# Kernel tuning notes

Hardware: AMD Instinct MI355X
Metric: run time of the kernel (lower is better)

The kernel has to match this reference:

```python
import jax, jax.numpy as jnp
import numpy as np

INPUT_DIM = 1024
OUTPUT_DIM = 1024
DEGREE = 3


def setup_inputs() -> dict:
    key = jax.random.key(0)
    kx, kc = jax.random.split(key)
    x = jax.random.normal(kx, (8192, INPUT_DIM), dtype=jnp.float32)
    std = 1.0 / (INPUT_DIM * (DEGREE + 1))
    bessel_coeffs = std * jax.random.normal(kc, (INPUT_DIM, OUTPUT_DIM, DEGREE + 1), dtype=jnp.float32)
    return {"x": x, "bessel_coeffs": bessel_coeffs}


def reference(x, bessel_coeffs):
    # x: [B, I]; bessel_coeffs: [I, O, D+1]
    degree = bessel_coeffs.shape[-1] - 1
    x = jnp.tanh(x.reshape(-1, bessel_coeffs.shape[0]))
    # Bessel-polynomial-like recurrence: b0 = 1, b1 = x + 1,
    # b_i = (2i-1)*x*b_{i-1} + b_{i-2}
    basis = [jnp.ones_like(x)]
    if degree > 0:
        basis.append(x + 1.0)
    for i in range(2, degree + 1):
        basis.append((2 * i - 1) * x * basis[i - 1] + basis[i - 2])
    bessel = jnp.stack(basis, axis=-1)  # [B, I, D+1]
    y = jnp.einsum("bid,iod->bo", bessel, bessel_coeffs)
    return y
```

## Files before the change

### kernel.cpp

```cpp
#include <hip/hip_runtime.h>
#include <hip/hip_bf16.h>
#include <cstdint>
#include <cstddef>


#define BATCH   8192
#define IN_DIM  1024
#define OUT_DIM 1024
#define KB      3072
#define NT      24
#define BM      128
#define BN      128
#define BUFB    32768

#define SA1 56.307f
#define SA2 127.0f
#define SA3 124.534f
#define TB1 12783.33f
#define TB2 5667.68f
#define TB3 5779.91f
#define INV_S 1.389284e-6f

typedef __attribute__((ext_vector_type(4))) int   i32x4;

static __device__ __forceinline__ int q8(float v) {
    int q = __float2int_rn(v);
    return q < -127 ? -127 : (q > 127 ? 127 : q);
}

__global__ __launch_bounds__(256) void prep_basis(const float* __restrict__ x,
                                                  int8_t* __restrict__ Aq) {
    int idx = blockIdx.x * 256 + threadIdx.x;
    int b = idx >> 8;
    int i = (idx & 255) << 2;
    const float4 xv = *reinterpret_cast<const float4*>(&x[(size_t)b * IN_DIM + i]);
    float xs[4] = {xv.x, xv.y, xv.z, xv.w};
    int w1 = 0, w2 = 0, w3 = 0;
#pragma unroll
    for (int j = 0; j < 4; ++j) {
        float t  = tanhf(xs[j]);
        float t2 = t * t;
        float t3 = t2 * t;
        w1 |= (q8(SA1 * t)  & 0xff) << (8 * j);
        w2 |= (q8(SA2 * t2) & 0xff) << (8 * j);
        w3 |= (q8(SA3 * t3) & 0xff) << (8 * j);
    }
    int* row = (int*)(Aq + (size_t)b * KB);
    int c = i >> 2;
    row[c]       = w1;
    row[256 + c] = w2;
    row[512 + c] = w3;
}

__global__ __launch_bounds__(256) void prep_coeffs(const float* __restrict__ C,
                                                   int8_t* __restrict__ Bq,
                                                   float* __restrict__ bias) {
    __shared__ int8_t tile[3][32][33];
    __shared__ float red[8][32];
    const int i0 = blockIdx.x * 32;
    const int o0 = blockIdx.y * 32;
    const int t  = threadIdx.x;
    const int lo = t & 31;
    const int li = t >> 5;
    float part = 0.0f;
#pragma unroll
    for (int r = 0; r < 4; ++r) {
        int i = li + r * 8;
        const float4 c4 = *reinterpret_cast<const float4*>(
            &C[((size_t)(i0 + i) * OUT_DIM + (o0 + lo)) * 4]);
        tile[0][i][lo] = (int8_t)q8(TB1 * (c4.y + 3.0f * c4.z + 6.0f * c4.w));
        tile[1][i][lo] = (int8_t)q8(TB2 * (3.0f * c4.z + 15.0f * c4.w));
        tile[2][i][lo] = (int8_t)q8(TB3 * (15.0f * c4.w));
        part += c4.x + c4.y + c4.z + c4.w;
    }
    red[li][lo] = part;
    __syncthreads();
#pragma unroll
    for (int r = 0; r < 4; ++r) {
        int o = (t >> 5) + r * 8;
        int i = t & 31;
#pragma unroll
        for (int d = 0; d < 3; ++d)
            Bq[(size_t)(o0 + o) * KB + d * IN_DIM + (i0 + i)] = tile[d][i][o];
    }
    if (t < 32) {
        float s = 0.0f;
#pragma unroll
        for (int k = 0; k < 8; ++k) s += red[k][t];
        atomicAdd(&bias[o0 + t], s);
    }
}

__global__ __launch_bounds__(256, 2) void gemm_kan(
    const int8_t* __restrict__ Aq,
    const int8_t* __restrict__ Bq,
    const float* __restrict__ bias,
    float* __restrict__ out)
{
    extern __shared__ char smem[];

    const int tid  = threadIdx.x;
    const int lane = tid & 63;
    const int wid  = tid >> 6;
    const int wm   = wid >> 1;
    const int wn   = wid & 1;

    const int bid  = blockIdx.x;
    const int xcd  = bid & 7;
    const int j    = bid >> 3;
    const int brow = ((xcd >> 1) * 16 + (j >> 2)) * BM;
    const int bcol = ((xcd & 1) * 4 + (j & 3)) * BN;

    const int l15 = lane & 15, lh = lane >> 4, l7 = lane & 7;
    const int pc0 = lh ^ l7;
    const int pc1 = pc0 ^ 4;

    int aoff[4][2], boff[4][2];
#pragma unroll
    for (int mi = 0; mi < 4; ++mi) {
        int r = wm * 64 + mi * 16 + l15;
        aoff[mi][0] = r * 128 + pc0 * 16;
        aoff[mi][1] = r * 128 + pc1 * 16;
    }
#pragma unroll
    for (int ni = 0; ni < 4; ++ni) {
        int r = wn * 64 + ni * 16 + l15;
        boff[ni][0] = 16384 + r * 128 + pc0 * 16;
        boff[ni][1] = 16384 + r * 128 + pc1 * 16;
    }

    const int srow   = tid >> 3;
    const int schunk = (tid & 7) ^ (srow & 7);

#define STAGE(KT_TILE, P)                                                             \
    do {                                                                              \
        const int kt_ = (KT_TILE) * 128;                                              \
        char* lbase_ = smem + (P) * BUFB;                                             \
        _Pragma("unroll")                                                             \
        for (int s_ = 0; s_ < 4; ++s_) {                                              \
            __builtin_amdgcn_global_load_lds(                                         \
                (const __attribute__((address_space(1))) void*)(                      \
                    Aq + (size_t)(brow + s_ * 32 + srow) * KB + kt_ + schunk * 16),   \
                (__attribute__((address_space(3))) void*)(                            \
                    lbase_ + s_ * 4096 + tid * 16), 16, 0, 0);                        \
        }                                                                             \
        _Pragma("unroll")                                                             \
        for (int s_ = 0; s_ < 4; ++s_) {                                              \
            __builtin_amdgcn_global_load_lds(                                         \
                (const __attribute__((address_space(1))) void*)(                      \
                    Bq + (size_t)(bcol + s_ * 32 + srow) * KB + kt_ + schunk * 16),   \
                (__attribute__((address_space(3))) void*)(                            \
                    lbase_ + 16384 + s_ * 4096 + tid * 16), 16, 0, 0);                \
        }                                                                             \
    } while (0)

    i32x4 acc[4][4];
#pragma unroll
    for (int mi = 0; mi < 4; ++mi)
#pragma unroll
        for (int ni = 0; ni < 4; ++ni)
            acc[mi][ni] = (i32x4){0, 0, 0, 0};

    STAGE(0, 0);
    __syncthreads();

    for (int t = 0; t < NT; ++t) {
        const int p = t & 1;
        if (t + 1 < NT) STAGE(t + 1, p ^ 1);

        const char* lb = smem + p * BUFB;
        i32x4 af[4][2], bfr[4][2];
#pragma unroll
        for (int mi = 0; mi < 4; ++mi) {
            af[mi][0] = *reinterpret_cast<const i32x4*>(lb + aoff[mi][0]);
            af[mi][1] = *reinterpret_cast<const i32x4*>(lb + aoff[mi][1]);
        }
#pragma unroll
        for (int ni = 0; ni < 4; ++ni) {
            bfr[ni][0] = *reinterpret_cast<const i32x4*>(lb + boff[ni][0]);
            bfr[ni][1] = *reinterpret_cast<const i32x4*>(lb + boff[ni][1]);
        }
        __builtin_amdgcn_s_setprio(1);
#pragma unroll
        for (int kk = 0; kk < 2; ++kk)
#pragma unroll
            for (int mi = 0; mi < 4; ++mi)
#pragma unroll
                for (int ni = 0; ni < 4; ++ni)
                    acc[mi][ni] = __builtin_amdgcn_mfma_i32_16x16x64_i8(
                        af[mi][kk], bfr[ni][kk], acc[mi][ni], 0, 0, 0);
        __builtin_amdgcn_s_setprio(0);

        if (t + 1 < NT) __syncthreads();
    }
#undef STAGE

    float bv[4];
#pragma unroll
    for (int ni = 0; ni < 4; ++ni)
        bv[ni] = bias[bcol + wn * 64 + ni * 16 + l15];
#pragma unroll
    for (int mi = 0; mi < 4; ++mi) {
#pragma unroll
        for (int r = 0; r < 4; ++r) {
            int row = brow + wm * 64 + mi * 16 + (lane >> 4) * 4 + r;
            float* orow = out + (size_t)row * OUT_DIM + bcol + wn * 64 + l15;
#pragma unroll
            for (int ni = 0; ni < 4; ++ni)
                orow[ni * 16] = (float)acc[mi][ni][r] * INV_S + bv[ni];
        }
    }
}

extern "C" void kernel_launch(void* const* d_in, const int* in_sizes, int n_in,
                              void* d_out, int out_size, void* d_ws, size_t ws_size,
                              hipStream_t stream) {
    (void)in_sizes; (void)n_in; (void)out_size; (void)ws_size;
    const float* x      = (const float*)d_in[0];
    const float* coeffs = (const float*)d_in[1];
    float* out = (float*)d_out;

    char* ws = (char*)d_ws;
    int8_t* Aq  = (int8_t*)ws;
    int8_t* Bq  = (int8_t*)(ws + (size_t)BATCH * KB);
    float* bias = (float*)(ws + (size_t)BATCH * KB + (size_t)OUT_DIM * KB);

    hipFuncSetAttribute((const void*)gemm_kan,
                        hipFuncAttributeMaxDynamicSharedMemorySize, 2 * BUFB);

    hipMemsetAsync(bias, 0, OUT_DIM * sizeof(float), stream);
    hipLaunchKernelGGL(prep_basis, dim3(BATCH * IN_DIM / 4 / 256), dim3(256), 0, stream,
                       x, Aq);
    hipLaunchKernelGGL(prep_coeffs, dim3(IN_DIM / 32, OUT_DIM / 32), dim3(256), 0, stream,
                       coeffs, Bq, bias);
    hipLaunchKernelGGL(gemm_kan, dim3((BATCH / BM) * (OUT_DIM / BN)), dim3(256),
                       2 * BUFB, stream,
                       Aq, Bq, bias, out);
}
```

Baseline: 53.74 us.

## Merge basis and coeff prep kernels, use fast tanh, widen per-thread work

Replaces the two preprocessing kernels with one launch whose blocks branch on block index into basis quantization or coefficient transpose-quantization. The basis path now handles 8 elements per thread with int2 stores, and computes tanh with exp plus a hardware reciprocal instead of tanhf. This saves one kernel launch and lets the two memory-bound prep jobs overlap on the device. The cheaper tanh may shift int8 rounding slightly, and the coefficient blocks now need shared memory that the basis blocks also reserve.

Result: faster. 49.47 us (median of 2 runs) (-7.9%).

```diff
diff --git a/kernel.cpp b/kernel.cpp
--- a/kernel.cpp
+++ b/kernel.cpp
@@ -12,6 +12,7 @@
 #define BM      128
 #define BN      128
 #define BUFB    32768
+#define NB_BASIS 4096
 
 #define SA1 56.307f
 #define SA2 127.0f
@@ -21,73 +22,83 @@
 #define TB3 5779.91f
 #define INV_S 1.389284e-6f
 
-typedef __attribute__((ext_vector_type(4))) int   i32x4;
+typedef __attribute__((ext_vector_type(4))) int i32x4;
 
 static __device__ __forceinline__ int q8(float v) {
     int q = __float2int_rn(v);
     return q < -127 ? -127 : (q > 127 ? 127 : q);
 }
 
-__global__ __launch_bounds__(256) void prep_basis(const float* __restrict__ x,
-                                                  int8_t* __restrict__ Aq) {
-    int idx = blockIdx.x * 256 + threadIdx.x;
-    int b = idx >> 8;
-    int i = (idx & 255) << 2;
-    const float4 xv = *reinterpret_cast<const float4*>(&x[(size_t)b * IN_DIM + i]);
-    float xs[4] = {xv.x, xv.y, xv.z, xv.w};
-    int w1 = 0, w2 = 0, w3 = 0;
-#pragma unroll
-    for (int j = 0; j < 4; ++j) {
-        float t  = tanhf(xs[j]);
-        float t2 = t * t;
-        float t3 = t2 * t;
-        w1 |= (q8(SA1 * t)  & 0xff) << (8 * j);
-        w2 |= (q8(SA2 * t2) & 0xff) << (8 * j);
-        w3 |= (q8(SA3 * t3) & 0xff) << (8 * j);
-    }
-    int* row = (int*)(Aq + (size_t)b * KB);
-    int c = i >> 2;
-    row[c]       = w1;
-    row[256 + c] = w2;
-    row[512 + c] = w3;
-}
-
-__global__ __launch_bounds__(256) void prep_coeffs(const float* __restrict__ C,
-                                                   int8_t* __restrict__ Bq,
-                                                   float* __restrict__ bias) {
-    __shared__ int8_t tile[3][32][33];
-    __shared__ float red[8][32];
-    const int i0 = blockIdx.x * 32;
-    const int o0 = blockIdx.y * 32;
-    const int t  = threadIdx.x;
-    const int lo = t & 31;
-    const int li = t >> 5;
-    float part = 0.0f;
-#pragma unroll
-    for (int r = 0; r < 4; ++r) {
-        int i = li + r * 8;
-        const float4 c4 = *reinterpret_cast<const float4*>(
-            &C[((size_t)(i0 + i) * OUT_DIM + (o0 + lo)) * 4]);
-        tile[0][i][lo] = (int8_t)q8(TB1 * (c4.y + 3.0f * c4.z + 6.0f * c4.w));
-        tile[1][i][lo] = (int8_t)q8(TB2 * (3.0f * c4.z + 15.0f * c4.w));
-        tile[2][i][lo] = (int8_t)q8(TB3 * (15.0f * c4.w));
-        part += c4.x + c4.y + c4.z + c4.w;
-    }
-    red[li][lo] = part;
-    __syncthreads();
-#pragma unroll
-    for (int r = 0; r < 4; ++r) {
-        int o = (t >> 5) + r * 8;
-        int i = t & 31;
-#pragma unroll
-        for (int d = 0; d < 3; ++d)
-            Bq[(size_t)(o0 + o) * KB + d * IN_DIM + (i0 + i)] = tile[d][i][o];
-    }
-    if (t < 32) {
-        float s = 0.0f;
-#pragma unroll
-        for (int k = 0; k < 8; ++k) s += red[k][t];
-        atomicAdd(&bias[o0 + t], s);
+static __device__ __forceinline__ float fast_tanh(float x) {
+    float e = __expf(2.0f * x);
+    return 1.0f - 2.0f * __builtin_amdgcn_rcpf(e + 1.0f);
+}
+
+__global__ __launch_bounds__(256) void prep_all(const float* __restrict__ x,
+                                                const float* __restrict__ C,
+                                                int8_t* __restrict__ Aq,
+                                                int8_t* __restrict__ Bq,
+                                                float* __restrict__ bias) {
+    const int t = threadIdx.x;
+    if (blockIdx.x < NB_BASIS) {
+        int idx = blockIdx.x * 256 + t;
+        int b = idx >> 7;
+        int i = (idx & 127) << 3;
+        const float* xr = x + (size_t)b * IN_DIM + i;
+        const float4 v0 = *reinterpret_cast<const float4*>(xr);
+        const float4 v1 = *reinterpret_cast<const float4*>(xr + 4);
+        float xs[8] = {v0.x, v0.y, v0.z, v0.w, v1.x, v1.y, v1.z, v1.w};
+        int w1[2] = {0, 0}, w2[2] = {0, 0}, w3[2] = {0, 0};
+#pragma unroll
+        for (int j = 0; j < 8; ++j) {
+            float tv = fast_tanh(xs[j]);
+            float t2 = tv * tv;
+            float t3 = t2 * tv;
+            int h = j >> 2, s = 8 * (j & 3);
+            w1[h] |= (q8(SA1 * tv) & 0xff) << s;
+            w2[h] |= (q8(SA2 * t2) & 0xff) << s;
+            w3[h] |= (q8(SA3 * t3) & 0xff) << s;
+        }
+        int* row = (int*)(Aq + (size_t)b * KB);
+        int c = i >> 2;
+        *reinterpret_cast<int2*>(&row[c])       = make_int2(w1[0], w1[1]);
+        *reinterpret_cast<int2*>(&row[256 + c]) = make_int2(w2[0], w2[1]);
+        *reinterpret_cast<int2*>(&row[512 + c]) = make_int2(w3[0], w3[1]);
+    } else {
+        __shared__ int8_t tile[3][32][33];
+        __shared__ float red[8][32];
+        const int cb = blockIdx.x - NB_BASIS;
+        const int i0 = (cb & 31) * 32;
+        const int o0 = (cb >> 5) * 32;
+        const int lo = t & 31;
+        const int li = t >> 5;
+        float part = 0.0f;
+#pragma unroll
+        for (int r = 0; r < 4; ++r) {
+            int i = li + r * 8;
+            const float4 c4 = *reinterpret_cast<const float4*>(
+                &C[((size_t)(i0 + i) * OUT_DIM + (o0 + lo)) * 4]);
+            tile[0][i][lo] = (int8_t)q8(TB1 * (c4.y + 3.0f * c4.z + 6.0f * c4.w));
+            tile[1][i][lo] = (int8_t)q8(TB2 * (3.0f * c4.z + 15.0f * c4.w));
+            tile[2][i][lo] = (int8_t)q8(TB3 * (15.0f * c4.w));
+            part += c4.x + c4.y + c4.z + c4.w;
+        }
+        red[li][lo] = part;
+        __syncthreads();
+#pragma unroll
+        for (int r = 0; r < 4; ++r) {
+            int o = (t >> 5) + r * 8;
+            int i = t & 31;
+#pragma unroll
+            for (int d = 0; d < 3; ++d)
+                Bq[(size_t)(o0 + o) * KB + d * IN_DIM + (i0 + i)] = tile[d][i][o];
+        }
+        if (t < 32) {
+            float s = 0.0f;
+#pragma unroll
+            for (int k = 0; k < 8; ++k) s += red[k][t];
+            atomicAdd(&bias[o0 + t], s);
+        }
     }
 }
 
@@ -229,10 +240,8 @@
                         hipFuncAttributeMaxDynamicSharedMemorySize, 2 * BUFB);
 
     hipMemsetAsync(bias, 0, OUT_DIM * sizeof(float), stream);
-    hipLaunchKernelGGL(prep_basis, dim3(BATCH * IN_DIM / 4 / 256), dim3(256), 0, stream,
-                       x, Aq);
-    hipLaunchKernelGGL(prep_coeffs, dim3(IN_DIM / 32, OUT_DIM / 32), dim3(256), 0, stream,
-                       coeffs, Bq, bias);
+    hipLaunchKernelGGL(prep_all, dim3(NB_BASIS + 1024), dim3(256), 0, stream,
+                       x, coeffs, Aq, Bq, bias);
     hipLaunchKernelGGL(gemm_kan, dim3((BATCH / BM) * (OUT_DIM / BN)), dim3(256),
                        2 * BUFB, stream,
                        Aq, Bq, bias, out);
```
